# Performance work log

Hardware: AMD Instinct MI355X
Metric: run time of the kernel (lower is better)

## Reference

```python
import jax, jax.numpy as jnp
import numpy as np

NHEAD, DK, DV, DMODEL, L = 8, 64, 64, 512, 32

def setup_inputs() -> dict:
    key = jax.random.key(0)
    ks = jax.random.split(key, 9)
    B, N = 4, 2048
    s = 1.0 / np.sqrt(DMODEL)
    return {
        "q": jax.random.normal(ks[0], (B, N, DMODEL), jnp.float32),
        "k": jax.random.normal(ks[1], (B, N, DMODEL), jnp.float32),
        "v": jax.random.normal(ks[2], (B, N, DMODEL), jnp.float32),
        "Wq": jax.random.normal(ks[3], (DMODEL, NHEAD * DK), jnp.float32) * s,
        "Wk": jax.random.normal(ks[4], (DMODEL, NHEAD * DK), jnp.float32) * s,
        "Wv": jax.random.normal(ks[5], (DMODEL, NHEAD * DV), jnp.float32) * s,
        "Wfc": jax.random.normal(ks[6], (NHEAD * DV, DMODEL), jnp.float32) * s,
        "ln_g": jnp.ones((DMODEL,), jnp.float32),
        "ln_b": jnp.zeros((DMODEL,), jnp.float32),
    }

def reference(q, k, v, Wq, Wk, Wv, Wfc, ln_g, ln_b):
    B, Nq, _ = q.shape
    residual = q
    # project and split heads: [B, H, N, d]
    qh = (q @ Wq).reshape(B, Nq, NHEAD, DK).transpose(0, 2, 1, 3)
    kh = (k @ Wk).reshape(B, k.shape[1], NHEAD, DK).transpose(0, 2, 1, 3)
    vh = (v @ Wv).reshape(B, v.shape[1], NHEAD, DV).transpose(0, 2, 1, 3)
    # scaled dot-product scores and softmax over keys
    attn = jnp.einsum('bhqd,bhkd->bhqk', qh / jnp.sqrt(jnp.float32(DK)), kh)
    attn = jax.nn.softmax(attn, axis=-1)
    # AWG: keep entries >= l-th largest per row, renormalize
    threshold = jax.lax.top_k(attn, L)[0][..., -1:]  # [B,H,Nq,1]
    W = jnp.where(attn >= threshold, attn, 0.0)
    W_out = W / jnp.sum(W, axis=-1, keepdims=True)
    out = jnp.einsum('bhqk,bhkd->bhqd', W_out, vh)
    out = out.transpose(0, 2, 1, 3).reshape(B, Nq, NHEAD * DV)
    out = out @ Wfc + residual
    # LayerNorm, eps=1e-6
    mu = jnp.mean(out, axis=-1, keepdims=True)
    var = jnp.var(out, axis=-1, keepdims=True)
    return (out - mu) / jnp.sqrt(var + 1e-6) * ln_g + ln_b
```

## Files before the change

### kernel.cpp

```cpp
#include <hip/hip_runtime.h>
#include <hip/hip_fp16.h>

#define BATCH 4
#define NSEQ 2048
#define DMODEL 512
#define NHEAD 8
#define HDIM 64
#define LSEL 32
#define MAXL 64
#define QROWS 16
#define CSTRIDE 331

typedef __attribute__((ext_vector_type(8))) _Float16 f16x8;
typedef __attribute__((ext_vector_type(4))) float f32x4;
typedef unsigned long long ull;

__device__ inline ushort f2h(float x) { __half h = __float2half(x); return *reinterpret_cast<ushort*>(&h); }
__device__ inline float h16f(ushort u) { __half t; *reinterpret_cast<ushort*>(&t) = u; return __half2float(t); }
__device__ inline float sort2f(uint su) {
    ushort hb = (su & 0x8000u) ? (ushort)(su ^ 0x8000u) : (ushort)(su ^ 0xFFFFu);
    return h16f(hb);
}
__device__ inline uint sm2(uint w) {
    uint s = (w >> 15) & 0x00010001u;
    uint m = (s << 15) - s;
    return w ^ (m | 0x80008000u);
}

__global__ __launch_bounds__(256) void cvtA_kernel(
    const float* __restrict__ q, const float* __restrict__ k, const float* __restrict__ v,
    ushort* __restrict__ q16, ushort* __restrict__ k16, ushort* __restrict__ v16)
{
    const int z = blockIdx.y;
    const float* src = (z == 0) ? q : (z == 1) ? k : v;
    ushort* dst = (z == 0) ? q16 : (z == 1) ? k16 : v16;
    const size_t base = (size_t)blockIdx.x * 2048 + threadIdx.x * 4;
    float4 fa = *(const float4*)(src + base);
    float4 fb = *(const float4*)(src + base + 1024);
    ushort4 ha = {f2h(fa.x), f2h(fa.y), f2h(fa.z), f2h(fa.w)};
    ushort4 hb = {f2h(fb.x), f2h(fb.y), f2h(fb.z), f2h(fb.w)};
    *(ushort4*)(dst + base) = ha;
    *(ushort4*)(dst + base + 1024) = hb;
}

__global__ __launch_bounds__(256) void cvtW_kernel(
    const float* __restrict__ Wq, const float* __restrict__ Wk,
    const float* __restrict__ Wv, const float* __restrict__ Wfc,
    ushort* __restrict__ Wt)
{
    const int z = blockIdx.y;
    const float* W = (z == 0) ? Wq : (z == 1) ? Wk : (z == 2) ? Wv : Wfc;
    ushort* O = Wt + (size_t)z * DMODEL * DMODEL;
    const int gt = blockIdx.x * 256 + threadIdx.x;
    const int n = gt & 511;
    const int kc = (gt >> 9) * 16;
    uint pk[8];
#pragma unroll
    for (int i = 0; i < 8; ++i) {
        uint lo = f2h(W[(size_t)(kc + 2 * i) * DMODEL + n]);
        uint hi = f2h(W[(size_t)(kc + 2 * i + 1) * DMODEL + n]);
        pk[i] = lo | (hi << 16);
    }
    uint4 u0 = {pk[0], pk[1], pk[2], pk[3]};
    uint4 u1 = {pk[4], pk[5], pk[6], pk[7]};
    *(uint4*)(O + (size_t)n * DMODEL + kc) = u0;
    *(uint4*)(O + (size_t)n * DMODEL + kc + 8) = u1;
}

template<int MODE>
__global__ __launch_bounds__(256, 2) void hgemm_kernel(
    const ushort* __restrict__ A0, const ushort* __restrict__ A1, const ushort* __restrict__ A2,
    const ushort* __restrict__ Wt,
    ushort* __restrict__ O0, ushort* __restrict__ O1, ushort* __restrict__ O2,
    float* __restrict__ Ofc)
{
    __shared__ ushort Ah[64][40];
    __shared__ ushort Bh[512][40];

    const int tid = threadIdx.x;
    const int wave = tid >> 6, lane = tid & 63;
    const int lr = lane & 15, lg = lane >> 4;
    const int bm = blockIdx.x * 64;
    const int z = blockIdx.y;

    const ushort* A16 = (MODE == 0) ? (z == 0 ? A0 : z == 1 ? A1 : A2) : A0;
    const ushort* Wz = Wt + (size_t)((MODE == 0) ? z : 3) * (DMODEL * DMODEL);

    f32x4 acc[4][8];
#pragma unroll
    for (int i = 0; i < 4; ++i)
#pragma unroll
        for (int j = 0; j < 8; ++j) acc[i][j] = (f32x4){0.f, 0.f, 0.f, 0.f};

    const int sar = tid >> 2, sak = (tid & 3) * 8;

    for (int k0 = 0; k0 < DMODEL; k0 += 32) {
        __syncthreads();
        *(uint4*)&Ah[sar][sak] = *(const uint4*)(A16 + (size_t)(bm + sar) * DMODEL + k0 + sak);
#pragma unroll
        for (int i = 0; i < 8; ++i) {
            int n = sar + 64 * i;
            *(uint4*)&Bh[n][sak] = *(const uint4*)(Wz + (size_t)n * DMODEL + k0 + sak);
        }
        __syncthreads();
        f16x8 af[4];
#pragma unroll
        for (int fr = 0; fr < 4; ++fr) af[fr] = *(const f16x8*)&Ah[fr * 16 + lr][lg * 8];
#pragma unroll
        for (int fc2 = 0; fc2 < 8; ++fc2) {
            f16x8 bf = *(const f16x8*)&Bh[wave * 128 + fc2 * 16 + lr][lg * 8];
#pragma unroll
            for (int fr = 0; fr < 4; ++fr)
                acc[fr][fc2] = __builtin_amdgcn_mfma_f32_16x16x32_f16(af[fr], bf, acc[fr][fc2], 0, 0, 0);
        }
    }

    if (MODE == 1) {
#pragma unroll
        for (int fr = 0; fr < 4; ++fr)
#pragma unroll
            for (int fc2 = 0; fc2 < 8; ++fc2)
#pragma unroll
                for (int r = 0; r < 4; ++r)
                    Ofc[(size_t)(bm + fr * 16 + lg * 4 + r) * DMODEL + wave * 128 + fc2 * 16 + lr] = acc[fr][fc2][r];
        return;
    }

    const float osc = (z == 0) ? 0.125f : 1.0f;
    ushort* O = (z == 0) ? O0 : (z == 1) ? O1 : O2;
    const int b = bm >> 11;
    const int nseq0 = bm & (NSEQ - 1);
    ushort* smw = (ushort*)&Bh[0][0] + wave * (64 * 72);
#pragma unroll
    for (int hp = 0; hp < 2; ++hp) {
        __syncthreads();
#pragma unroll
        for (int f4 = 0; f4 < 4; ++f4) {
            int fc2 = hp * 4 + f4;
            int nl = f4 * 16 + lr;
#pragma unroll
            for (int fr = 0; fr < 4; ++fr)
#pragma unroll
                for (int r = 0; r < 4; ++r)
                    smw[(fr * 16 + lg * 4 + r) * 72 + nl] = f2h(acc[fr][fc2][r] * osc);
        }
        __syncthreads();
        const int h = wave * 2 + hp;
        ushort* obase = O + ((size_t)(b * NHEAD + h) * NSEQ + nseq0) * HDIM;
#pragma unroll
        for (int i = 0; i < 8; ++i) {
            int m = i * 8 + (lane >> 3);
            int dc = (lane & 7) * 8;
            *(uint4*)(obase + (size_t)m * HDIM + dc) = *(const uint4*)(smw + m * 72 + dc);
        }
    }
}

__device__ inline int wave_sum6(int c) {
    int tot = (int)__popcll(__ballot(c & 1));
    tot += (int)__popcll(__ballot(c & 2)) << 1;
    tot += (int)__popcll(__ballot(c & 4)) << 2;
    tot += (int)__popcll(__ballot(c & 8)) << 3;
    tot += (int)__popcll(__ballot(c & 16)) << 4;
    tot += (int)__popcll(__ballot(c & 32)) << 5;
    return tot;
}

__device__ uint full_thr(const ushort* Sr, int lane, uint lo0) {
    uint flo = lo0, fhi = 0xFFFFu;
#pragma unroll 1
    for (int it2 = 0; it2 < 16; ++it2) {
        uint mid = (flo + fhi + 1) >> 1, M = mid << 16;
        int cl = 0;
#pragma unroll
        for (int it = 0; it < 4; ++it) {
            uint4 r4 = *(const uint4*)(Sr + it * 512 + lane * 8);
            cl += ((r4.x << 16) >= M) + ((r4.x & 0xFFFF0000u) >= M);
            cl += ((r4.y << 16) >= M) + ((r4.y & 0xFFFF0000u) >= M);
            cl += ((r4.z << 16) >= M) + ((r4.z & 0xFFFF0000u) >= M);
            cl += ((r4.w << 16) >= M) + ((r4.w & 0xFFFF0000u) >= M);
        }
        bool ge = wave_sum6(cl) >= LSEL;
        flo = ge ? mid : flo;
        fhi = ge ? fhi : mid - 1;
    }
    return flo;
}

__device__ int recount(const ushort* Sr, int lane, uint th) {
    int cs = 0;
#pragma unroll
    for (int it = 0; it < 4; ++it) {
        uint4 r4 = *(const uint4*)(Sr + it * 512 + lane * 8);
        cs += ((r4.x << 16) >= th) + ((r4.x & 0xFFFF0000u) >= th);
        cs += ((r4.y << 16) >= th) + ((r4.y & 0xFFFF0000u) >= th);
        cs += ((r4.z << 16) >= th) + ((r4.z & 0xFFFF0000u) >= th);
        cs += ((r4.w << 16) >= th) + ((r4.w & 0xFFFF0000u) >= th);
    }
    return cs;
}

__device__ float extract_big(const ushort* Sr, int lane, uint th, float Mv,
                             int pre, uint* selrow)
{
    const float L2E = 1.4426950408889634f;
    float wp = 0.f;
    int pos = pre;
#pragma unroll
    for (int it = 0; it < 4; ++it) {
        uint4 r4 = *(const uint4*)(Sr + it * 512 + lane * 8);
        uint ib = (uint)(it * 512 + lane * 8);
        uint wds[4] = {r4.x, r4.y, r4.z, r4.w};
#pragma unroll
        for (int c = 0; c < 4; ++c) {
            uint vL = wds[c] << 16, vH = wds[c] & 0xFFFF0000u;
            if (vL >= th) {
                ushort w16 = f2h(exp2f((sort2f(vL >> 16) - Mv) * L2E));
                if (pos < MAXL) { selrow[pos] = ((uint)w16 << 16) | (ib + c * 2); wp += h16f(w16); }
                ++pos;
            }
            if (vH >= th) {
                ushort w16 = f2h(exp2f((sort2f(vH >> 16) - Mv) * L2E));
                if (pos < MAXL) { selrow[pos] = ((uint)w16 << 16) | (ib + c * 2 + 1); wp += h16f(w16); }
                ++pos;
            }
        }
    }
#pragma unroll
    for (int off = 32; off >= 1; off >>= 1) wp += __shfl_xor(wp, off);
    return wp;
}

#define INS5(T0, T1, T2, T3, T4, P) { \
    uint m1_ = min(P, T0); T0 = max(P, T0); \
    uint m2_ = min(m1_, T1); T1 = max(m1_, T1); \
    uint m3_ = min(m2_, T2); T2 = max(m2_, T2); \
    uint m4_ = min(m3_, T3); T3 = max(m3_, T3); \
    T4 = max(m4_, T4); }

template<int PH>
__global__ __launch_bounds__(512, 4) void attn_kernel(
    const ushort* __restrict__ qh, const ushort* __restrict__ kh,
    const ushort* __restrict__ vh, ushort* __restrict__ ao)
{
    __shared__ uint cand[QROWS * CSTRIDE];
    __shared__ __align__(16) uint sel[QROWS][MAXL];
    __shared__ __align__(16) ushort Sb1[2056];
    __shared__ float wsums[QROWS];
    __shared__ int   nks[QROWS];
    __shared__ int   missflag[QROWS];

    const int tid = threadIdx.x;
    const int wave = tid >> 6;
    const int lane = tid & 63;

    const int wid = blockIdx.y * gridDim.x + blockIdx.x;
    const int cpx = (gridDim.x * gridDim.y) >> 3;
    const int flat = (wid & 7) * cpx + (wid >> 3);
    const int bh = flat >> 7;
    const int q0 = (flat & 127) * QROWS;

    const int lr = lane & 15;
    const int lg = lane >> 4;
    const float L2E = 1.4426950408889634f;

    const ushort* Qb = qh + ((size_t)bh * NSEQ + q0) * HDIM;
    const ushort* Kb = kh + (size_t)bh * NSEQ * HDIM;

    f16x8 qf0 = *(const f16x8*)(Qb + lr * HDIM + lg * 8);
    f16x8 qf1 = *(const f16x8*)(Qb + lr * HDIM + 32 + lg * 8);

    uint sA0 = 0, sA1 = 0, sA2 = 0, sA3 = 0, sA4 = 0;
    uint sB0 = 0, sB1 = 0, sB2 = 0, sB3 = 0, sB4 = 0;
    float csum = 0.f;

    const int kwbase = wave * 256;
    const ushort* kp = Kb + (size_t)kwbase * HDIM + lr * HDIM + lg * 8;
    f16x8 a0 = *(const f16x8*)kp;
    f16x8 a1 = *(const f16x8*)(kp + 32);

#pragma unroll
    for (int t = 0; t < 16; ++t) {
        f16x8 n0 = a0, n1 = a1;
        if (t < 15) {
            n0 = *(const f16x8*)(kp + 1024);
            n1 = *(const f16x8*)(kp + 1056);
        }
        f32x4 acc = {0.f, 0.f, 0.f, 0.f};
        acc = __builtin_amdgcn_mfma_f32_16x16x32_f16(a0, qf0, acc, 0, 0, 0);
        acc = __builtin_amdgcn_mfma_f32_16x16x32_f16(a1, qf1, acc, 0, 0, 0);
        if constexpr (PH == 0) {
            csum += acc[0] + acc[1] + acc[2] + acc[3];
        } else {
            const uint col = (uint)(kwbase + t * 16 + lg * 4);
            uint w0 = (uint)f2h(acc[0]) | ((uint)f2h(acc[1]) << 16);
            uint w1 = (uint)f2h(acc[2]) | ((uint)f2h(acc[3]) << 16);
            w0 = sm2(w0); w1 = sm2(w1);
            uint p;
            p = (w0 << 16) | col;               INS5(sA0, sA1, sA2, sA3, sA4, p);
            p = (w0 & 0xFFFF0000u) | (col + 1); INS5(sA0, sA1, sA2, sA3, sA4, p);
            p = (w1 << 16) | (col + 2);         INS5(sB0, sB1, sB2, sB3, sB4, p);
            p = (w1 & 0xFFFF0000u) | (col + 3); INS5(sB0, sB1, sB2, sB3, sB4, p);
        }
        a0 = n0; a1 = n1;
        kp += 1024;
    }

    if constexpr (PH == 0) {
        ((uint*)ao)[(size_t)wid * 512 + tid] = (uint)f2h(csum);
        return;
    }

    {
        const int sid = wave * 8 + lg * 2;
        const int cb = lr * CSTRIDE + sid;
        cand[cb +   0] = sA0; cand[cb +  66] = sA1; cand[cb + 132] = sA2;
        cand[cb + 198] = sA3; cand[cb + 264] = sA4;
        cand[cb +   1] = sB0; cand[cb +  67] = sB1; cand[cb + 133] = sB2;
        cand[cb + 199] = sB3; cand[cb + 265] = sB4;
    }
    __syncthreads();

    if constexpr (PH == 1) {
        uint cs2 = sA0 ^ sA1 ^ sA2 ^ sA3 ^ sA4 ^ sB0 ^ sB1 ^ sB2 ^ sB3 ^ sB4;
        cs2 ^= cand[(wave * 64 + lane) & 1023];
        ((uint*)ao)[(size_t)wid * 512 + tid] = cs2;
        return;
    }

    const int halfid = lane >> 5;
    const int s = lane & 31;
    const int qr = wave * 2 + halfid;
    const int b = bh >> 3, hh = bh & 7;
    const ull LOMASK = 0xFFFFFFFFull;
    const ull HB = halfid ? ~LOMASK : LOMASK;

    uint c0, c1, c2, c3, c4, c5, c6, c7, c8, c9;
    {
        const int cb = qr * CSTRIDE + s;
        c0 = cand[cb];       c1 = cand[cb +  66]; c2 = cand[cb + 132];
        c3 = cand[cb + 198]; c4 = cand[cb + 264];
        c5 = cand[cb + 32];       c6 = cand[cb +  66 + 32]; c7 = cand[cb + 132 + 32];
        c8 = cand[cb + 198 + 32]; c9 = cand[cb + 264 + 32];
    }

    uint mx = max(c0, c5);
#pragma unroll
    for (int off = 1; off <= 16; off <<= 1) mx = max(mx, (uint)__shfl_xor((int)mx, off));
    const float Mv = sort2f(mx >> 16);

    uint lo = 0, hi = 0xFFFFu;
#pragma unroll
    for (int it = 0; it < 16; ++it) {
        uint mid = (lo + hi + 1) >> 1, M = mid << 16;
        int cnt = (c0 >= M) + (c1 >= M) + (c2 >= M) + (c3 >= M) + (c4 >= M)
                + (c5 >= M) + (c6 >= M) + (c7 >= M) + (c8 >= M) + (c9 >= M);
        ull m0 = __ballot(cnt & 1), m1 = __ballot(cnt & 2);
        ull m2 = __ballot(cnt & 4), m3 = __ballot(cnt & 8);
        int tH = (int)__popcll(m0 & HB) + 2 * (int)__popcll(m1 & HB)
               + 4 * (int)__popcll(m2 & HB) + 8 * (int)__popcll(m3 & HB);
        bool ge = tH >= LSEL;
        lo = ge ? mid : lo;
        hi = ge ? hi : mid - 1;
    }
    const uint th = lo << 16;

    ull mm = __ballot((c4 >= th) || (c9 >= th));
    const bool missMy = (mm & HB) != 0ull;

    if (!missMy) {
        int csel = (c0 >= th) + (c1 >= th) + (c2 >= th) + (c3 >= th)
                 + (c5 >= th) + (c6 >= th) + (c7 >= th) + (c8 >= th);
        ull below = ((1ull << lane) - 1ull) & HB;
        int pre = 0, tot = 0;
#pragma unroll
        for (int bb = 0; bb < 4; ++bb) {
            ull m = __ballot((csel >> bb) & 1);
            pre += (int)__popcll(m & below) << bb;
            tot += (int)__popcll(m & HB) << bb;
        }
        uint regs[8] = {c0, c1, c2, c3, c5, c6, c7, c8};
        float wp = 0.f;
        int k2 = 0;
#pragma unroll
        for (int i = 0; i < 8; ++i) {
            uint ui = regs[i];
            if (ui >= th) {
                ushort w16 = f2h(exp2f((sort2f(ui >> 16) - Mv) * L2E));
                int pos = pre + k2;
                if (pos < MAXL) { sel[qr][pos] = ((uint)w16 << 16) | (ui & 0xFFFFu); wp += h16f(w16); }
                ++k2;
            }
        }
#pragma unroll
        for (int off = 1; off <= 16; off <<= 1) wp += __shfl_xor(wp, off);
        if (s == 0) { wsums[qr] = wp; nks[qr] = (tot < MAXL) ? tot : MAXL; }
    }
    if (s == 0) missflag[qr] = missMy ? 1 : 0;
    __syncthreads();

    for (int r = 0; r < QROWS; ++r) {
        if (missflag[r]) {
            __syncthreads();
#pragma unroll 4
            for (int t = 0; t < 16; ++t) {
                const ushort* Kt = Kb + (size_t)(kwbase + t * 16) * HDIM;
                f16x8 ra0 = *(const f16x8*)(Kt + lr * HDIM + lg * 8);
                f16x8 ra1 = *(const f16x8*)(Kt + lr * HDIM + 32 + lg * 8);
                f32x4 ac2 = {0.f, 0.f, 0.f, 0.f};
                ac2 = __builtin_amdgcn_mfma_f32_16x16x32_f16(ra0, qf0, ac2, 0, 0, 0);
                ac2 = __builtin_amdgcn_mfma_f32_16x16x32_f16(ra1, qf1, ac2, 0, 0, 0);
                if (lr == r) {
                    uint w0 = (uint)f2h(ac2[0]) | ((uint)f2h(ac2[1]) << 16);
                    uint w1 = (uint)f2h(ac2[2]) | ((uint)f2h(ac2[3]) << 16);
                    uint2 pk = {sm2(w0), sm2(w1)};
                    *(uint2*)&Sb1[kwbase + t * 16 + lg * 4] = pk;
                }
            }
            __syncthreads();
            if (wave == (r >> 1)) {
                const int h = r & 1;
                const float Mvr = __shfl(Mv, h * 32);
                const uint lor = (uint)__shfl((int)lo, h * 32);
                uint ft = full_thr(Sb1, lane, lor);
                uint thv = ft << 16;
                int cs = recount(Sb1, lane, thv);
                ull below64 = (1ull << lane) - 1ull;
                int preS = 0, totS = 0;
#pragma unroll
                for (int bb = 0; bb < 6; ++bb) {
                    ull m = __ballot((cs >> bb) & 1);
                    preS += (int)__popcll(m & below64) << bb;
                    totS += (int)__popcll(m) << bb;
                }
                float wr = extract_big(Sb1, lane, thv, Mvr, preS, &sel[r][0]);
                if (lane == 0) { wsums[r] = wr; nks[r] = (totS < MAXL) ? totS : MAXL; }
            }
        }
    }
    __syncthreads();

    const __half2* V2 = reinterpret_cast<const __half2*>(vh + (size_t)bh * NSEQ * HDIM);
    const int dp = lane & 31;
    const int nkMy = nks[qr];
    const float wsMy = wsums[qr];
    const uint* selp = &sel[qr][0];

    float ox = 0.f, oy = 0.f;
    int j = 0;
    for (; j + 8 <= nkMy; j += 8) {
        uint e[8];
        *(uint4*)&e[0] = *(const uint4*)(selp + j);
        *(uint4*)&e[4] = *(const uint4*)(selp + j + 4);
        float2 vv[8];
        float ww[8];
#pragma unroll
        for (int i2 = 0; i2 < 8; ++i2) {
            int idx = (int)(e[i2] & 0xFFFFu);
            ww[i2] = h16f((ushort)(e[i2] >> 16));
            vv[i2] = __half22float2(V2[(size_t)idx * 32 + dp]);
        }
#pragma unroll
        for (int i2 = 0; i2 < 8; ++i2) { ox += ww[i2] * vv[i2].x; oy += ww[i2] * vv[i2].y; }
    }
    for (; j < nkMy; ++j) {
        uint e = selp[j];
        int idx = (int)(e & 0xFFFFu);
        float w = h16f((ushort)(e >> 16));
        float2 v0 = __half22float2(V2[(size_t)idx * 32 + dp]);
        ox += w * v0.x; oy += w * v0.y;
    }

    const float inv = 1.f / wsMy;
    uint opk = (uint)f2h(ox * inv) | ((uint)f2h(oy * inv) << 16);
    *(uint*)(ao + ((size_t)(b * NSEQ) + q0 + qr) * DMODEL + hh * HDIM + dp * 2) = opk;
}

__global__ __launch_bounds__(256) void ln_kernel(
    const float* __restrict__ fcr, const float* __restrict__ resid,
    const float* __restrict__ g, const float* __restrict__ bta, float* __restrict__ out)
{
    const int row = blockIdx.x * 4 + (threadIdx.x >> 6);
    const int lane = threadIdx.x & 63;
    const size_t base = (size_t)row * DMODEL + lane * 8;
    float4 xa = *(const float4*)(fcr + base);
    float4 xb = *(const float4*)(fcr + base + 4);
    float4 ra = *(const float4*)(resid + base);
    float4 rb = *(const float4*)(resid + base + 4);
    xa.x += ra.x; xa.y += ra.y; xa.z += ra.z; xa.w += ra.w;
    xb.x += rb.x; xb.y += rb.y; xb.z += rb.z; xb.w += rb.w;
    float sum = xa.x + xa.y + xa.z + xa.w + xb.x + xb.y + xb.z + xb.w;
    float sq = xa.x * xa.x + xa.y * xa.y + xa.z * xa.z + xa.w * xa.w
             + xb.x * xb.x + xb.y * xb.y + xb.z * xb.z + xb.w * xb.w;
#pragma unroll
    for (int off = 32; off >= 1; off >>= 1) {
        sum += __shfl_xor(sum, off);
        sq += __shfl_xor(sq, off);
    }
    float mean = sum * (1.f / 512.f);
    float var = sq * (1.f / 512.f) - mean * mean;
    float rstd = rsqrtf(var + 1e-6f);
    float4 ga = *(const float4*)(g + lane * 8);
    float4 gb = *(const float4*)(g + lane * 8 + 4);
    float4 ba = *(const float4*)(bta + lane * 8);
    float4 bb = *(const float4*)(bta + lane * 8 + 4);
    float4 oa, ob;
    oa.x = (xa.x - mean) * rstd * ga.x + ba.x;
    oa.y = (xa.y - mean) * rstd * ga.y + ba.y;
    oa.z = (xa.z - mean) * rstd * ga.z + ba.z;
    oa.w = (xa.w - mean) * rstd * ga.w + ba.w;
    ob.x = (xb.x - mean) * rstd * gb.x + bb.x;
    ob.y = (xb.y - mean) * rstd * gb.y + bb.y;
    ob.z = (xb.z - mean) * rstd * gb.z + bb.z;
    ob.w = (xb.w - mean) * rstd * gb.w + bb.w;
    *(float4*)(out + base) = oa;
    *(float4*)(out + base + 4) = ob;
}

extern "C" void kernel_launch(void* const* d_in, const int* in_sizes, int n_in,
                              void* d_out, int out_size, void* d_ws, size_t ws_size,
                              hipStream_t stream)
{
    (void)in_sizes; (void)n_in; (void)out_size; (void)ws_size;

    const float* q   = (const float*)d_in[0];
    const float* k   = (const float*)d_in[1];
    const float* v   = (const float*)d_in[2];
    const float* Wq  = (const float*)d_in[3];
    const float* Wk  = (const float*)d_in[4];
    const float* Wv  = (const float*)d_in[5];
    const float* Wfc = (const float*)d_in[6];
    const float* g   = (const float*)d_in[7];
    const float* b   = (const float*)d_in[8];
    float* out = (float*)d_out;

    const size_t SZ = (size_t)BATCH * NSEQ * DMODEL;
    const size_t WSZ = (size_t)DMODEL * DMODEL;
    ushort* w16 = (ushort*)d_ws;
    ushort* q16 = w16;
    ushort* k16 = w16 + SZ;
    ushort* v16 = w16 + 2 * SZ;
    ushort* Wt  = w16 + 3 * SZ;
    ushort* qh  = Wt + 4 * WSZ;
    ushort* kh  = qh + SZ;
    ushort* vh  = kh + SZ;
    ushort* ao  = vh + SZ;
    float* fc_raw = (float*)d_ws;

    cvtA_kernel<<<dim3(2048, 3), 256, 0, stream>>>(q, k, v, q16, k16, v16);
    cvtW_kernel<<<dim3(64, 4), 256, 0, stream>>>(Wq, Wk, Wv, Wfc, Wt);
    hgemm_kernel<0><<<dim3(128, 3), 256, 0, stream>>>(q16, k16, v16, Wt, qh, kh, vh, nullptr);
    attn_kernel<0><<<dim3(128, 8), 512, 0, stream>>>(qh, kh, vh, ao);
    attn_kernel<1><<<dim3(128, 8), 512, 0, stream>>>(qh, kh, vh, ao);
    attn_kernel<2><<<dim3(NSEQ / QROWS, BATCH * NHEAD), 512, 0, stream>>>(qh, kh, vh, ao);
    hgemm_kernel<1><<<dim3(128, 1), 256, 0, stream>>>(ao, nullptr, nullptr, Wt, nullptr, nullptr, nullptr, fc_raw);
    ln_kernel<<<(BATCH * NSEQ) / 4, 256, 0, stream>>>(fc_raw, q, g, b, out);
}
```

Measured before the change: 373.1 us.

## Drop probe attention launches and process two query tiles per block

Removes the two diagnostic attention launches (PH=0 checksum and PH=1 candidate-only) that did redundant QK work. Restructures the attention kernel so each block handles 32 query rows as two 16-row tiles sharing the same K head, halving the grid. Candidates for the first tile are held in registers while the second tile's scores are computed, which raises register pressure. The tail phases then run back-to-back per tile.

```diff
diff --git a/kernel.cpp b/kernel.cpp
--- a/kernel.cpp
+++ b/kernel.cpp
@@ -238,41 +238,12 @@
     uint m4_ = min(m3_, T3); T3 = max(m3_, T3); \
     T4 = max(m4_, T4); }
 
-template<int PH>
-__global__ __launch_bounds__(512, 4) void attn_kernel(
-    const ushort* __restrict__ qh, const ushort* __restrict__ kh,
-    const ushort* __restrict__ vh, ushort* __restrict__ ao)
-{
-    __shared__ uint cand[QROWS * CSTRIDE];
-    __shared__ __align__(16) uint sel[QROWS][MAXL];
-    __shared__ __align__(16) ushort Sb1[2056];
-    __shared__ float wsums[QROWS];
-    __shared__ int   nks[QROWS];
-    __shared__ int   missflag[QROWS];
-
-    const int tid = threadIdx.x;
-    const int wave = tid >> 6;
-    const int lane = tid & 63;
-
-    const int wid = blockIdx.y * gridDim.x + blockIdx.x;
-    const int cpx = (gridDim.x * gridDim.y) >> 3;
-    const int flat = (wid & 7) * cpx + (wid >> 3);
-    const int bh = flat >> 7;
-    const int q0 = (flat & 127) * QROWS;
-
-    const int lr = lane & 15;
-    const int lg = lane >> 4;
-    const float L2E = 1.4426950408889634f;
-
-    const ushort* Qb = qh + ((size_t)bh * NSEQ + q0) * HDIM;
-    const ushort* Kb = kh + (size_t)bh * NSEQ * HDIM;
-
-    f16x8 qf0 = *(const f16x8*)(Qb + lr * HDIM + lg * 8);
-    f16x8 qf1 = *(const f16x8*)(Qb + lr * HDIM + 32 + lg * 8);
-
+__device__ __forceinline__ void p1_run(int lane, int wave,
+    const ushort* __restrict__ Kb, f16x8 qf0, f16x8 qf1, uint* cand)
+{
+    const int lr = lane & 15, lg = lane >> 4;
     uint sA0 = 0, sA1 = 0, sA2 = 0, sA3 = 0, sA4 = 0;
     uint sB0 = 0, sB1 = 0, sB2 = 0, sB3 = 0, sB4 = 0;
-    float csum = 0.f;
 
     const int kwbase = wave * 256;
     const ushort* kp = Kb + (size_t)kwbase * HDIM + lr * HDIM + lg * 8;
@@ -289,60 +260,44 @@
         f32x4 acc = {0.f, 0.f, 0.f, 0.f};
         acc = __builtin_amdgcn_mfma_f32_16x16x32_f16(a0, qf0, acc, 0, 0, 0);
         acc = __builtin_amdgcn_mfma_f32_16x16x32_f16(a1, qf1, acc, 0, 0, 0);
-        if constexpr (PH == 0) {
-            csum += acc[0] + acc[1] + acc[2] + acc[3];
-        } else {
-            const uint col = (uint)(kwbase + t * 16 + lg * 4);
-            uint w0 = (uint)f2h(acc[0]) | ((uint)f2h(acc[1]) << 16);
-            uint w1 = (uint)f2h(acc[2]) | ((uint)f2h(acc[3]) << 16);
-            w0 = sm2(w0); w1 = sm2(w1);
-            uint p;
-            p = (w0 << 16) | col;               INS5(sA0, sA1, sA2, sA3, sA4, p);
-            p = (w0 & 0xFFFF0000u) | (col + 1); INS5(sA0, sA1, sA2, sA3, sA4, p);
-            p = (w1 << 16) | (col + 2);         INS5(sB0, sB1, sB2, sB3, sB4, p);
-            p = (w1 & 0xFFFF0000u) | (col + 3); INS5(sB0, sB1, sB2, sB3, sB4, p);
-        }
+        const uint col = (uint)(kwbase + t * 16 + lg * 4);
+        uint w0 = (uint)f2h(acc[0]) | ((uint)f2h(acc[1]) << 16);
+        uint w1 = (uint)f2h(acc[2]) | ((uint)f2h(acc[3]) << 16);
+        w0 = sm2(w0); w1 = sm2(w1);
+        uint p;
+        p = (w0 << 16) | col;               INS5(sA0, sA1, sA2, sA3, sA4, p);
+        p = (w0 & 0xFFFF0000u) | (col + 1); INS5(sA0, sA1, sA2, sA3, sA4, p);
+        p = (w1 << 16) | (col + 2);         INS5(sB0, sB1, sB2, sB3, sB4, p);
+        p = (w1 & 0xFFFF0000u) | (col + 3); INS5(sB0, sB1, sB2, sB3, sB4, p);
         a0 = n0; a1 = n1;
         kp += 1024;
     }
 
-    if constexpr (PH == 0) {
-        ((uint*)ao)[(size_t)wid * 512 + tid] = (uint)f2h(csum);
-        return;
-    }
-
-    {
-        const int sid = wave * 8 + lg * 2;
-        const int cb = lr * CSTRIDE + sid;
-        cand[cb +   0] = sA0; cand[cb +  66] = sA1; cand[cb + 132] = sA2;
-        cand[cb + 198] = sA3; cand[cb + 264] = sA4;
-        cand[cb +   1] = sB0; cand[cb +  67] = sB1; cand[cb + 133] = sB2;
-        cand[cb + 199] = sB3; cand[cb + 265] = sB4;
-    }
-    __syncthreads();
-
-    if constexpr (PH == 1) {
-        uint cs2 = sA0 ^ sA1 ^ sA2 ^ sA3 ^ sA4 ^ sB0 ^ sB1 ^ sB2 ^ sB3 ^ sB4;
-        cs2 ^= cand[(wave * 64 + lane) & 1023];
-        ((uint*)ao)[(size_t)wid * 512 + tid] = cs2;
-        return;
-    }
-
+    const int sid = wave * 8 + lg * 2;
+    const int cb = lr * CSTRIDE + sid;
+    cand[cb +   0] = sA0; cand[cb +  66] = sA1; cand[cb + 132] = sA2;
+    cand[cb + 198] = sA3; cand[cb + 264] = sA4;
+    cand[cb +   1] = sB0; cand[cb +  67] = sB1; cand[cb + 133] = sB2;
+    cand[cb + 199] = sB3; cand[cb + 265] = sB4;
+}
+
+__device__ __forceinline__ void p2_tail(
+    uint c0, uint c1, uint c2, uint c3, uint c4,
+    uint c5, uint c6, uint c7, uint c8, uint c9,
+    int lane, int wave, int bh, int q0,
+    f16x8 qf0, f16x8 qf1,
+    const ushort* __restrict__ Kb, const ushort* __restrict__ vh,
+    ushort* __restrict__ ao,
+    uint (*sel)[MAXL], ushort* Sb1, float* wsums, int* nks, int* missflag)
+{
+    const float L2E = 1.4426950408889634f;
+    const int lr = lane & 15, lg = lane >> 4;
     const int halfid = lane >> 5;
     const int s = lane & 31;
     const int qr = wave * 2 + halfid;
     const int b = bh >> 3, hh = bh & 7;
     const ull LOMASK = 0xFFFFFFFFull;
     const ull HB = halfid ? ~LOMASK : LOMASK;
-
-    uint c0, c1, c2, c3, c4, c5, c6, c7, c8, c9;
-    {
-        const int cb = qr * CSTRIDE + s;
-        c0 = cand[cb];       c1 = cand[cb +  66]; c2 = cand[cb + 132];
-        c3 = cand[cb + 198]; c4 = cand[cb + 264];
-        c5 = cand[cb + 32];       c6 = cand[cb +  66 + 32]; c7 = cand[cb + 132 + 32];
-        c8 = cand[cb + 198 + 32]; c9 = cand[cb + 264 + 32];
-    }
 
     uint mx = max(c0, c5);
 #pragma unroll
@@ -399,6 +354,7 @@
     if (s == 0) missflag[qr] = missMy ? 1 : 0;
     __syncthreads();
 
+    const int kwbase = wave * 256;
     for (int r = 0; r < QROWS; ++r) {
         if (missflag[r]) {
             __syncthreads();
@@ -476,6 +432,77 @@
     *(uint*)(ao + ((size_t)(b * NSEQ) + q0 + qr) * DMODEL + hh * HDIM + dp * 2) = opk;
 }
 
+__global__ __launch_bounds__(512, 4) void attn_kernel(
+    const ushort* __restrict__ qh, const ushort* __restrict__ kh,
+    const ushort* __restrict__ vh, ushort* __restrict__ ao)
+{
+    __shared__ uint cand[QROWS * CSTRIDE];
+    __shared__ __align__(16) uint sel[QROWS][MAXL];
+    __shared__ __align__(16) ushort Sb1[2056];
+    __shared__ float wsums[QROWS];
+    __shared__ int   nks[QROWS];
+    __shared__ int   missflag[QROWS];
+
+    const int tid = threadIdx.x;
+    const int wave = tid >> 6;
+    const int lane = tid & 63;
+
+    const int wid = blockIdx.y * gridDim.x + blockIdx.x;
+    const int cpx = (gridDim.x * gridDim.y) >> 3;
+    const int flat = (wid & 7) * cpx + (wid >> 3);
+    const int bh = flat >> 6;
+    const int q00 = (flat & 63) * 32;
+    const int q01 = q00 + QROWS;
+
+    const int lr = lane & 15;
+    const int lg = lane >> 4;
+
+    const ushort* Kb = kh + (size_t)bh * NSEQ * HDIM;
+    const ushort* Qb0 = qh + ((size_t)bh * NSEQ + q00) * HDIM;
+    const ushort* Qb1 = Qb0 + QROWS * HDIM;
+
+    f16x8 qa0 = *(const f16x8*)(Qb0 + lr * HDIM + lg * 8);
+    f16x8 qa1 = *(const f16x8*)(Qb0 + lr * HDIM + 32 + lg * 8);
+    f16x8 qb0 = *(const f16x8*)(Qb1 + lr * HDIM + lg * 8);
+    f16x8 qb1 = *(const f16x8*)(Qb1 + lr * HDIM + 32 + lg * 8);
+
+    p1_run(lane, wave, Kb, qa0, qa1, cand);
+    __syncthreads();
+
+    uint e0, e1, e2, e3, e4, e5, e6, e7, e8, e9;
+    {
+        const int halfid = lane >> 5, s = lane & 31;
+        const int qr = wave * 2 + halfid;
+        const int cb = qr * CSTRIDE + s;
+        e0 = cand[cb];       e1 = cand[cb +  66]; e2 = cand[cb + 132];
+        e3 = cand[cb + 198]; e4 = cand[cb + 264];
+        e5 = cand[cb + 32];       e6 = cand[cb +  66 + 32]; e7 = cand[cb + 132 + 32];
+        e8 = cand[cb + 198 + 32]; e9 = cand[cb + 264 + 32];
+    }
+    __syncthreads();
+
+    p1_run(lane, wave, Kb, qb0, qb1, cand);
+    __syncthreads();
+
+    uint f0, f1, f2, f3, f4, f5, f6, f7, f8, f9;
+    {
+        const int halfid = lane >> 5, s = lane & 31;
+        const int qr = wave * 2 + halfid;
+        const int cb = qr * CSTRIDE + s;
+        f0 = cand[cb];       f1 = cand[cb +  66]; f2 = cand[cb + 132];
+        f3 = cand[cb + 198]; f4 = cand[cb + 264];
+        f5 = cand[cb + 32];       f6 = cand[cb +  66 + 32]; f7 = cand[cb + 132 + 32];
+        f8 = cand[cb + 198 + 32]; f9 = cand[cb + 264 + 32];
+    }
+
+    p2_tail(e0, e1, e2, e3, e4, e5, e6, e7, e8, e9,
+            lane, wave, bh, q00, qa0, qa1, Kb, vh, ao,
+            sel, Sb1, wsums, nks, missflag);
+    p2_tail(f0, f1, f2, f3, f4, f5, f6, f7, f8, f9,
+            lane, wave, bh, q01, qb0, qb1, Kb, vh, ao,
+            sel, Sb1, wsums, nks, missflag);
+}
+
 __global__ __launch_bounds__(256) void ln_kernel(
     const float* __restrict__ fcr, const float* __restrict__ resid,
     const float* __restrict__ g, const float* __restrict__ bta, float* __restrict__ out)
@@ -550,9 +577,7 @@
     cvtA_kernel<<<dim3(2048, 3), 256, 0, stream>>>(q, k, v, q16, k16, v16);
     cvtW_kernel<<<dim3(64, 4), 256, 0, stream>>>(Wq, Wk, Wv, Wfc, Wt);
     hgemm_kernel<0><<<dim3(128, 3), 256, 0, stream>>>(q16, k16, v16, Wt, qh, kh, vh, nullptr);
-    attn_kernel<0><<<dim3(128, 8), 512, 0, stream>>>(qh, kh, vh, ao);
-    attn_kernel<1><<<dim3(128, 8), 512, 0, stream>>>(qh, kh, vh, ao);
-    attn_kernel<2><<<dim3(NSEQ / QROWS, BATCH * NHEAD), 512, 0, stream>>>(qh, kh, vh, ao);
+    attn_kernel<<<dim3(64, 32), 512, 0, stream>>>(qh, kh, vh, ao);
     hgemm_kernel<1><<<dim3(128, 1), 256, 0, stream>>>(ao, nullptr, nullptr, Wt, nullptr, nullptr, nullptr, fc_raw);
     ln_kernel<<<(BATCH * NSEQ) / 4, 256, 0, stream>>>(fc_raw, q, g, b, out);
 }
```

Result: faster. 359.5 us (-3.6%).
